# Kernel optimization log

Measured on AMD Instinct MI355X. Metric: run time of the kernel, lower is better.

The kernel has to match this reference:

```python
import jax, jax.numpy as jnp
import numpy as np

N_HEADS = 8
NODE_DIM, EDGE_DIM, TIME_DIM = 172, 172, 100
OUT_DIM = NODE_DIM + TIME_DIM  # 272, divisible by N_HEADS -> pad_dim = 0
HEAD_DIM = OUT_DIM // N_HEADS  # 34
KEY_DIM = NODE_DIM + EDGE_DIM + TIME_DIM  # 444
B, NBR = 4096, 64
LN_EPS = 1e-5


def setup_inputs() -> dict:
    key = jax.random.key(0)
    ks = jax.random.split(key, 12)
    s = 0.02
    return {
        "node_feat": jax.random.normal(ks[0], (B, NODE_DIM), jnp.float32),
        "time_feat": jax.random.normal(ks[1], (B, 1, TIME_DIM), jnp.float32),
        "edge_feat": jax.random.normal(ks[2], (B, NBR, EDGE_DIM), jnp.float32),
        "nbr_node_feat": jax.random.normal(ks[3], (B, NBR, NODE_DIM), jnp.float32),
        "nbr_time_feat": jax.random.normal(ks[4], (B, NBR, TIME_DIM), jnp.float32),
        "nbr_mask": jax.random.randint(ks[5], (B, NBR), 0, 2, jnp.int32),
        "W_Q": jax.random.normal(ks[6], (OUT_DIM, OUT_DIM), jnp.float32) * s,
        "W_KV": jax.random.normal(ks[7], (2 * OUT_DIM, KEY_DIM), jnp.float32) * s,
        "W_O": jax.random.normal(ks[8], (OUT_DIM, OUT_DIM), jnp.float32) * s,
        "b_O": jax.random.normal(ks[9], (OUT_DIM,), jnp.float32) * s,
        "ln_gamma": jnp.ones((OUT_DIM,), jnp.float32),
        "ln_beta": jnp.zeros((OUT_DIM,), jnp.float32),
    }


def reference(node_feat, time_feat, edge_feat, nbr_node_feat, nbr_time_feat,
              nbr_mask, W_Q, W_KV, W_O, b_O, ln_gamma, ln_beta):
    # Query/residual: concat node + time features -> (B, out_dim) (L=1 squeezed)
    R = jnp.concatenate([node_feat, time_feat[:, 0, :]], axis=-1)  # (B, D)
    Q = R @ W_Q.T  # (B, D)
    # Keys/values from neighbors
    Z_in = jnp.concatenate([nbr_node_feat, edge_feat, nbr_time_feat], axis=-1)  # (B,N,key_dim)
    Z = jnp.einsum('bnk,dk->bnd', Z_in, W_KV)  # (B, N, 2D)
    K, V = Z[..., :OUT_DIM], Z[..., OUT_DIM:]
    # Split heads
    Qh = Q.reshape(B, N_HEADS, HEAD_DIM)              # (B,H,d)
    Kh = K.reshape(B, NBR, N_HEADS, HEAD_DIM)         # (B,N,H,d)
    Vh = V.reshape(B, NBR, N_HEADS, HEAD_DIM)
    # Single-query attention scores: (B,H,N)
    scores = jnp.einsum('bhd,bnhd->bhn', Qh, Kh) * (HEAD_DIM ** -0.5)
    pad = (nbr_mask == 0)[:, None, :]  # (B,1,N)
    scores = jnp.where(pad, jnp.float32(-1e10), scores)
    A = jax.nn.softmax(scores, axis=-1)  # dropout is identity in eval / p=0
    O = jnp.einsum('bhn,bnhd->bhd', A, Vh).reshape(B, OUT_DIM)
    out = O @ W_O.T + b_O
    # Residual + LayerNorm
    x = out + R
    mu = jnp.mean(x, axis=-1, keepdims=True)
    var = jnp.mean(jnp.square(x - mu), axis=-1, keepdims=True)
    return (x - mu) * jax.lax.rsqrt(var + LN_EPS) * ln_gamma + ln_beta
```

## Files before the change

### kernel.cpp

```cpp
#include <hip/hip_runtime.h>
#include <hip/hip_bf16.h>
#include <string.h>

#define NROWS    4096
#define NBR      64
#define NODE_DIM 172
#define EDGE_DIM 172
#define TIME_DIM 100
#define OUT_DIM  272
#define KEY_DIM  444
#define KPAD     448
#define QK_PAD   320
#define N_HEADS  8
#define HEAD_DIM 34

typedef __attribute__((ext_vector_type(8))) short short8_t;
typedef __attribute__((ext_vector_type(4))) float f32x4;

__device__ inline short f2b(float x) {
  unsigned u = __builtin_bit_cast(unsigned, x);
  unsigned r = (u + 0x7fffu + ((u >> 16) & 1u)) >> 16;
  return (short)r;
}

__device__ inline unsigned pk2(float lo, float hi) {
  __hip_bfloat162 h = __float22bfloat162_rn(make_float2(lo, hi));
  unsigned u;
  memcpy(&u, &h, 4);
  return u;
}

typedef const __attribute__((address_space(1))) void gv_t;
typedef __attribute__((address_space(3))) void lv_t;
__device__ inline void gld16(const void* g, void* l) {
  __builtin_amdgcn_global_load_lds((gv_t*)g, (lv_t*)l, 16, 0, 0);
}

__device__ inline void barrier_lgkm() {
  asm volatile("s_waitcnt lgkmcnt(0)" ::: "memory");
  __builtin_amdgcn_sched_barrier(0);
  __builtin_amdgcn_s_barrier();
}

template<int ROWS, int KP, int K0>
__device__ inline void pad_rows(char* A, int t) {
  constexpr int NC8 = (KP - K0) / 4;
  constexpr int LPR = 512 / ROWS;
  int r = t / LPR;
  int j = t % LPR;
  char* Arow = A + r * (2 * KP);
  int swz = (r & 7) << 4;
  uint2 zz; zz.x = 0; zz.y = 0;
  for (int c8 = j; c8 < NC8; c8 += LPR)
    *(uint2*)(Arow + ((2 * K0 + 8 * c8) ^ swz)) = zz;
}

template<int MT, int KP, int NKK>
__device__ inline void gemm_tile(const short* __restrict__ Wrow, const char* A,
                                 int lr, int lk, f32x4* acc) {
#pragma unroll
  for (int kk = 0; kk < NKK; ++kk) {
    short8_t bfrag = *(const short8_t*)(Wrow + lr * KP + kk * 32 + lk * 8);
#pragma unroll
    for (int mt = 0; mt < MT; ++mt) {
      short8_t afrag = *(const short8_t*)(A + (mt * 16 + lr) * (2 * KP) +
                                          ((kk * 64 + lk * 16) ^ ((lr & 7) << 4)));
      acc[mt] = __builtin_amdgcn_mfma_f32_16x16x32_bf16(afrag, bfrag, acc[mt], 0, 0, 0);
    }
  }
}

__global__ void convert_w(const float* __restrict__ Wkv, const float* __restrict__ Wq,
                          const float* __restrict__ Wo, short* __restrict__ wq_b,
                          short* __restrict__ wo_b, short* __restrict__ wkt,
                          short* __restrict__ wvh) {
  int i = blockIdx.x * 256 + threadIdx.x;
  if (i < OUT_DIM * QK_PAD) {
    int r = i / QK_PAD, c = i - r * QK_PAD;
    wq_b[i] = (c < OUT_DIM) ? f2b(Wq[r * OUT_DIM + c]) : (short)0;
    wo_b[i] = (c < OUT_DIM) ? f2b(Wo[r * OUT_DIM + c]) : (short)0;
  }
  if (i < N_HEADS * 448 * 64) {
    int h = i / 28672;
    int rem = i - h * 28672;
    int n = rem >> 6, d = rem & 63;
    wkt[i] = (n < KEY_DIM && d < HEAD_DIM) ? f2b(Wkv[(h * HEAD_DIM + d) * KEY_DIM + n])
                                           : (short)0;
  }
  if (i < N_HEADS * 48 * 448) {
    int h = i / 21504;
    int rem = i - h * 21504;
    int cp = rem / 448, k = rem - cp * 448;
    wvh[i] = (cp < HEAD_DIM && k < KEY_DIM)
                 ? f2b(Wkv[(OUT_DIM + h * HEAD_DIM + cp) * KEY_DIM + k])
                 : (short)0;
  }
}

__global__ __launch_bounds__(512) void q_qt(const float* __restrict__ node_feat,
                                            const float* __restrict__ time_feat,
                                            const short* __restrict__ Wq,
                                            const short* __restrict__ Wkt,
                                            short* __restrict__ Qtg) {
  __shared__ char Rlds[16 * 640];
  __shared__ char Qp[16 * 1024];
  int rb = blockIdx.x * 16, t = threadIdx.x;
  {
    int r = t >> 5, j = t & 31;
    const float4* pn = (const float4*)(node_feat + (size_t)(rb + r) * NODE_DIM);
    const float4* pt = (const float4*)(time_feat + (size_t)(rb + r) * TIME_DIM);
    float4 vn[2], vt4;
    int in_[2], it_;
#pragma unroll
    for (int i = 0; i < 2; ++i) { int f = j + 32 * i; in_[i] = f > 42 ? 42 : f; vn[i] = pn[in_[i]]; }
    it_ = j > 24 ? 24 : j; vt4 = pt[it_];
    char* Arow = Rlds + r * 640;
    int swz = (r & 7) << 4;
#pragma unroll
    for (int i = 0; i < 2; ++i) {
      uint2 w; w.x = pk2(vn[i].x, vn[i].y); w.y = pk2(vn[i].z, vn[i].w);
      *(uint2*)(Arow + ((8 * in_[i]) ^ swz)) = w;
    }
    {
      uint2 w; w.x = pk2(vt4.x, vt4.y); w.y = pk2(vt4.z, vt4.w);
      *(uint2*)(Arow + ((344 + 8 * it_) ^ swz)) = w;
    }
    if (j < 12) { uint2 zz; zz.x = 0; zz.y = 0; *(uint2*)(Arow + ((544 + 8 * j) ^ swz)) = zz; }
  }
  {
    uint4 zz; zz.x = 0; zz.y = 0; zz.z = 0; zz.w = 0;
    for (int i = t; i < 1024; i += 512) ((uint4*)Qp)[i] = zz;
  }
  __syncthreads();
  int wave = t >> 6, lane = t & 63, lr = lane & 15, lk = lane >> 4;
  f32x4 z = {0.f, 0.f, 0.f, 0.f};

  for (int nt = wave; nt < 17; nt += 8) {
    int nb = nt * 16;
    f32x4 acc[1] = {z};
    gemm_tile<1, QK_PAD, QK_PAD / 32>(Wq + nb * QK_PAD, Rlds, lr, lk, acc);
    int c = nb + lr;
    int h = c / HEAD_DIM, d = c - h * HEAD_DIM;
#pragma unroll
    for (int e = 0; e < 4; ++e) {
      int r = lk * 4 + e;
      *(short*)(Qp + r * 1024 + h * 128 + ((2 * d) ^ ((r & 7) << 4))) = f2b(acc[0][e]);
    }
  }
  __syncthreads();

  int h = wave;
  const short* Wh = Wkt + h * 28672;
  for (int nt = 0; nt < 28; ++nt) {
    f32x4 acc = z;
#pragma unroll
    for (int kk = 0; kk < 2; ++kk) {
      short8_t bfrag = *(const short8_t*)(Wh + (nt * 16 + lr) * 64 + kk * 32 + lk * 8);
      short8_t afrag = *(const short8_t*)(Qp + lr * 1024 + h * 128 +
                                          ((kk * 64 + lk * 16) ^ ((lr & 7) << 4)));
      acc = __builtin_amdgcn_mfma_f32_16x16x32_bf16(afrag, bfrag, acc, 0, 0, 0);
    }
#pragma unroll
    for (int e = 0; e < 4; ++e) {
      int n = nt * 16 + lr;
      *(short*)((char*)Qtg + (size_t)(rb + lk * 4 + e) * 7168 + h * 896 +
                ((2 * n) ^ (h << 4))) = f2b(acc[e] * 0.17149858514250882f);
    }
  }
}

__device__ inline void stage_chunk(const float* __restrict__ nn,
                                   const float* __restrict__ ef,
                                   const float* __restrict__ tf,
                                   const short* __restrict__ Qtg,
                                   int b, int half, char* buf, char* qtslot, char* dump,
                                   int wave, int lane) {
  size_t row0 = (size_t)b * NBR + half * 32;
  const char* nb = (const char*)(nn + row0 * NODE_DIM);
  const char* eb = (const char*)(ef + row0 * EDGE_DIM);
  const char* tb = (const char*)(tf + row0 * TIME_DIM);
  const char* qb = (const char*)Qtg + (size_t)b * 7168;
#pragma unroll
  for (int i = 0; i < 8; ++i) {
    int q = wave * 8 + i;
    if (q < 22) {
      int off = q * 1024 + lane * 16; if (off > 22000) off = 22000;
      gld16(nb + off, buf + q * 1024);
    } else if (q < 44) {
      int off = (q - 22) * 1024 + lane * 16; if (off > 22000) off = 22000;
      gld16(eb + off, buf + 22528 + (q - 22) * 1024);
    } else if (q < 57) {
      int off = (q - 44) * 1024 + lane * 16; if (off > 12784) off = 12784;
      gld16(tb + off, buf + 45056 + (q - 44) * 1024);
    } else {
      int off = (q - 57) * 1024 + lane * 16;
      gld16(qb + off, half == 0 ? (qtslot + (q - 57) * 1024) : dump);
    }
  }
}

__global__ __launch_bounds__(512) void attn7(const float* __restrict__ nn,
                                             const float* __restrict__ ef,
                                             const float* __restrict__ tf,
                                             const int* __restrict__ nbr_mask,
                                             const short* __restrict__ Qtg,
                                             short* __restrict__ Yh2) {
  __shared__ char Zbuf[2][58368];
  __shared__ char QtS[2][7168];
  __shared__ char Dump[1024];
  __shared__ float Spart[4][32][8];
  __shared__ char Pb[16 * 64];
  __shared__ float Mh[8], Lh[8], Fh[8];
  __shared__ int Mlds[1024];
  int t = threadIdx.x;
  int wave = t >> 6, lane = t & 63, lr = lane & 15, lk = lane >> 4;
  int bbase = blockIdx.x * 16;
  f32x4 z = {0.f, 0.f, 0.f, 0.f};
  f32x4 accY[4] = {z, z, z, z};

  if (t < 256) ((int4*)Mlds)[t] = ((const int4*)(nbr_mask + (size_t)bbase * 64))[t];
  stage_chunk(nn, ef, tf, Qtg, bbase, 0, Zbuf[0], QtS[0], Dump, wave, lane);

  for (int ci = 0; ci < 32; ++ci) {
    int b = bbase + (ci >> 1), half = ci & 1;
    char* cur = Zbuf[ci & 1];

    if (ci < 31) {
      int b2 = bbase + ((ci + 1) >> 1);
      stage_chunk(nn, ef, tf, Qtg, b2, (ci + 1) & 1, Zbuf[(ci + 1) & 1], QtS[b2 & 1],
                  Dump, wave, lane);
      asm volatile("s_waitcnt vmcnt(8) lgkmcnt(0)" ::: "memory");
    } else {
      asm volatile("s_waitcnt vmcnt(0) lgkmcnt(0)" ::: "memory");
    }
    __builtin_amdgcn_sched_barrier(0);
    __builtin_amdgcn_s_barrier();

    int r = t >> 4, j = t & 15;
    f32x4 v[7];
#pragma unroll
    for (int i = 0; i < 7; ++i) {
      int k = j * 4 + i * 64;
      int off = (k < 172) ? (r * 688 + 4 * k)
              : (k < 344) ? (22528 + r * 688 + 4 * (k - 172))
                          : (45056 + r * 400 + 4 * (k - 344));
      v[i] = *(const f32x4*)(cur + off);
    }
    if (j == 15) { v[6][0] = 0.f; v[6][1] = 0.f; v[6][2] = 0.f; v[6][3] = 0.f; }
    barrier_lgkm();
    {
      char* Arow = cur + r * 896;
      int swz = (r & 7) << 4;
#pragma unroll
      for (int i = 0; i < 7; ++i) {
        uint2 w; w.x = pk2(v[i][0], v[i][1]); w.y = pk2(v[i][2], v[i][3]);
        *(uint2*)(Arow + ((8 * j + 128 * i) ^ swz)) = w;
      }
    }
    barrier_lgkm();

    {
      int ntl = wave & 1, kq = wave >> 1;
      int tb0 = kq < 2 ? kq * 4 : 8 + (kq - 2) * 3;
      int cnt = kq < 2 ? 4 : 3;
      f32x4 acc = z;
      const char* qbase = QtS[b & 1] + (lr & 7) * 896;
      const char* zbase = cur + (ntl * 16 + lr) * 896;
      int swz = (lr & 7) << 4;
      for (int it = 0; it < cnt; ++it) {
        int keb = 2 * ((tb0 + it) * 32 + lk * 8);
        short8_t a = *(const short8_t*)(qbase + (keb ^ swz));
        short8_t bb = *(const short8_t*)(zbase + (keb ^ swz));
        acc = __builtin_amdgcn_mfma_f32_16x16x32_bf16(a, bb, acc, 0, 0, 0);
      }
#pragma unroll
      for (int e = 0; e < 4; ++e) {
        int h = lk * 4 + e;
        if (h < 8) Spart[kq][ntl * 16 + lr][h] = acc[e];
      }
    }
    barrier_lgkm();

    {
      int h = wave, n = lane & 31;
      float s = Spart[0][n][h] + Spart[1][n][h] + Spart[2][n][h] + Spart[3][n][h];
      if (Mlds[(ci >> 1) * 64 + half * 32 + n] == 0) s = -1e10f;
      float m = s;
#pragma unroll
      for (int off = 16; off >= 1; off >>= 1) m = fmaxf(m, __shfl_xor(m, off));
      float mp = (half == 0) ? -3e38f : Mh[h];
      float mn = fmaxf(mp, m);
      float e = __expf(s - mn);
      float sum = e;
#pragma unroll
      for (int off = 16; off >= 1; off >>= 1) sum += __shfl_xor(sum, off);
      float f = __expf(mp - mn);
      if (lane == 0) {
        Lh[h] = (half ? Lh[h] : 0.f) * f + sum;
        Mh[h] = mn;
        Fh[h] = f;
      }
      int off2 = (2 * n) ^ ((h & 3) << 4);
      *(short*)(Pb + h * 64 + off2) = f2b(e);
      *(short*)(Pb + (h + 8) * 64 + off2) = 0;
    }
    barrier_lgkm();

    {
      short8_t pa = *(const short8_t*)(Pb + lr * 64 + ((lk * 16) ^ ((lr & 3) << 4)));
#pragma unroll
      for (int s7 = 0; s7 < 4; ++s7) {
        int vt = wave + 8 * s7;
        if (vt < 28) {
          int colb = 2 * (vt * 16 + lr);
          const char* zb_base = cur + (lk * 8) * 896;
          short8_t zb;
#pragma unroll
          for (int jx = 0; jx < 8; ++jx)
            zb[jx] = *(const short*)(zb_base + jx * 896 + (colb ^ (jx << 4)));
#pragma unroll
          for (int e = 0; e < 4; ++e) accY[s7][e] *= Fh[(lk * 4 + e) & 7];
          accY[s7] = __builtin_amdgcn_mfma_f32_16x16x32_bf16(pa, zb, accY[s7], 0, 0, 0);
        }
      }
      if (half == 1 && lk < 2) {
        float inv[4];
#pragma unroll
        for (int e = 0; e < 4; ++e) inv[e] = 1.f / Lh[lk * 4 + e];
#pragma unroll
        for (int s7 = 0; s7 < 4; ++s7) {
          int vt = wave + 8 * s7;
          if (vt < 28) {
            int k = vt * 16 + lr, kk2 = k >> 5, kp = k & 31;
#pragma unroll
            for (int e = 0; e < 4; ++e)
              Yh2[((size_t)((lk * 4 + e) * 14 + kk2) * 4096 + b) * 32 + kp] =
                  f2b(accY[s7][e] * inv[e]);
          }
        }
      }
    }
    __builtin_amdgcn_s_barrier();
  }
}

__global__ __launch_bounds__(512) void out_ln2(const short* __restrict__ Yh2,
                                               const short* __restrict__ Wvh,
                                               const short* __restrict__ Wo,
                                               const float* __restrict__ bO,
                                               const float* __restrict__ node_feat,
                                               const float* __restrict__ time_feat,
                                               const float* __restrict__ gamma,
                                               const float* __restrict__ beta,
                                               float* __restrict__ out) {
  __shared__ char Alds[16 * 640];
  __shared__ float X[16 * 276];
  int rb = blockIdx.x * 16;
  int t = threadIdx.x;
  int wave = t >> 6, lane = t & 63, lr = lane & 15, lk = lane >> 4;
  pad_rows<16, QK_PAD, OUT_DIM>(Alds, t);
  f32x4 z = {0.f, 0.f, 0.f, 0.f};

  for (int p = wave; p < 24; p += 8) {
    int h = p / 3, nt = p - h * 3;
    f32x4 acc = z;
#pragma unroll
    for (int kk = 0; kk < 14; ++kk) {
      short8_t bfrag = *(const short8_t*)(Wvh + h * 21504 + (nt * 16 + lr) * 448 +
                                          kk * 32 + lk * 8);
      short8_t afrag = *(const short8_t*)(
          Yh2 + ((size_t)(h * 14 + kk) * 4096 + rb + lr) * 32 + lk * 8);
      acc = __builtin_amdgcn_mfma_f32_16x16x32_bf16(afrag, bfrag, acc, 0, 0, 0);
    }
    int cl = nt * 16 + lr;
    if (cl < HEAD_DIM) {
      int c = h * HEAD_DIM + cl;
#pragma unroll
      for (int e = 0; e < 4; ++e) {
        int r = lk * 4 + e;
        *(short*)(Alds + r * 640 + ((2 * c) ^ ((r & 7) << 4))) = f2b(acc[e]);
      }
    }
  }
  __syncthreads();

  for (int nt = wave; nt < 17; nt += 8) {
    int nb = nt * 16;
    f32x4 acc[1] = {z};
    gemm_tile<1, QK_PAD, QK_PAD / 32>(Wo + nb * QK_PAD, Alds, lr, lk, acc);
    int c = nb + lr;
    float bo = bO[c];
#pragma unroll
    for (int e = 0; e < 4; ++e) {
      int r = lk * 4 + e;
      int gr = rb + r;
      float Rv = (c < NODE_DIM) ? node_feat[(size_t)gr * NODE_DIM + c]
                                : time_feat[(size_t)gr * TIME_DIM + (c - NODE_DIM)];
      X[r * 276 + c] = acc[0][e] + bo + Rv;
    }
  }
  __syncthreads();

  int row = t >> 5, j = t & 31;
  float s1 = 0.f, s2 = 0.f;
  for (int c = j; c < OUT_DIM; c += 32) {
    float v = X[row * 276 + c];
    s1 += v; s2 += v * v;
  }
#pragma unroll
  for (int off = 16; off >= 1; off >>= 1) {
    s1 += __shfl_xor(s1, off);
    s2 += __shfl_xor(s2, off);
  }
  float mu = s1 * (1.f / OUT_DIM);
  float var = s2 * (1.f / OUT_DIM) - mu * mu;
  float inv = rsqrtf(fmaxf(var, 0.f) + 1e-5f);
  int gr = rb + row;
  for (int c = j; c < OUT_DIM; c += 32) {
    float v = X[row * 276 + c];
    out[(size_t)gr * OUT_DIM + c] = (v - mu) * inv * gamma[c] + beta[c];
  }
}

extern "C" void kernel_launch(void* const* d_in, const int* in_sizes, int n_in,
                              void* d_out, int out_size, void* d_ws, size_t ws_size,
                              hipStream_t stream) {
  const float* node_feat = (const float*)d_in[0];
  const float* time_feat = (const float*)d_in[1];
  const float* edge_feat = (const float*)d_in[2];
  const float* nbr_node  = (const float*)d_in[3];
  const float* nbr_time  = (const float*)d_in[4];
  const int*   nbr_mask  = (const int*)d_in[5];
  const float* W_Q   = (const float*)d_in[6];
  const float* W_KV  = (const float*)d_in[7];
  const float* W_O   = (const float*)d_in[8];
  const float* b_O   = (const float*)d_in[9];
  const float* gamma = (const float*)d_in[10];
  const float* beta  = (const float*)d_in[11];
  float* out = (float*)d_out;
  char* ws = (char*)d_ws;

  short* wq_b = (short*)(ws);
  short* wo_b = (short*)(ws + 174080);
  short* wvh  = (short*)(ws + 348160);
  short* wkt  = (short*)(ws + 692224);
  short* Qtg  = (short*)(ws + 1150976);
  short* Yh2  = (short*)(ws + 30511104);

  convert_w<<<896, 256, 0, stream>>>(W_KV, W_Q, W_O, wq_b, wo_b, wkt, wvh);
  q_qt<<<NROWS / 16, 512, 0, stream>>>(node_feat, time_feat, wq_b, wkt, Qtg);
  attn7<<<256, 512, 0, stream>>>(nbr_node, edge_feat, nbr_time, nbr_mask, Qtg, Yh2);
  out_ln2<<<NROWS / 16, 512, 0, stream>>>(Yh2, wvh, wo_b, b_O, node_feat, time_feat,
                                          gamma, beta, out);
}
```

Before: 198.8 us.

## Replace persistent double-buffered attention kernel with one block per batch row

Replaces the persistent 256-block attention kernel, which double-buffered neighbor chunks and Qt tiles in LDS, with a 4096-block kernel that loads each half-chunk synchronously into a single LDS buffer. Qt is now stored unswizzled in global memory and read directly in the score MFMA loop, and the mask is read per lane from global. This cuts LDS use and may let more blocks share a CU, relying on occupancy rather than explicit prefetch to hide load latency. In exchange it gives up the intra-block load/compute overlap and adds global reads in the inner loop.

Result: faster. 190.0 us (-4.4%).

```diff
diff --git a/kernel.cpp b/kernel.cpp
--- a/kernel.cpp
+++ b/kernel.cpp
@@ -9,7 +9,6 @@
 #define TIME_DIM 100
 #define OUT_DIM  272
 #define KEY_DIM  444
-#define KPAD     448
 #define QK_PAD   320
 #define N_HEADS  8
 #define HEAD_DIM 34
@@ -34,12 +33,6 @@
 typedef __attribute__((address_space(3))) void lv_t;
 __device__ inline void gld16(const void* g, void* l) {
   __builtin_amdgcn_global_load_lds((gv_t*)g, (lv_t*)l, 16, 0, 0);
-}
-
-__device__ inline void barrier_lgkm() {
-  asm volatile("s_waitcnt lgkmcnt(0)" ::: "memory");
-  __builtin_amdgcn_sched_barrier(0);
-  __builtin_amdgcn_s_barrier();
 }
 
 template<int ROWS, int KP, int K0>
@@ -161,95 +154,66 @@
       acc = __builtin_amdgcn_mfma_f32_16x16x32_bf16(afrag, bfrag, acc, 0, 0, 0);
     }
 #pragma unroll
-    for (int e = 0; e < 4; ++e) {
-      int n = nt * 16 + lr;
-      *(short*)((char*)Qtg + (size_t)(rb + lk * 4 + e) * 7168 + h * 896 +
-                ((2 * n) ^ (h << 4))) = f2b(acc[e] * 0.17149858514250882f);
-    }
-  }
-}
-
-__device__ inline void stage_chunk(const float* __restrict__ nn,
-                                   const float* __restrict__ ef,
-                                   const float* __restrict__ tf,
-                                   const short* __restrict__ Qtg,
-                                   int b, int half, char* buf, char* qtslot, char* dump,
-                                   int wave, int lane) {
-  size_t row0 = (size_t)b * NBR + half * 32;
-  const char* nb = (const char*)(nn + row0 * NODE_DIM);
-  const char* eb = (const char*)(ef + row0 * EDGE_DIM);
-  const char* tb = (const char*)(tf + row0 * TIME_DIM);
-  const char* qb = (const char*)Qtg + (size_t)b * 7168;
-#pragma unroll
-  for (int i = 0; i < 8; ++i) {
-    int q = wave * 8 + i;
-    if (q < 22) {
-      int off = q * 1024 + lane * 16; if (off > 22000) off = 22000;
-      gld16(nb + off, buf + q * 1024);
-    } else if (q < 44) {
-      int off = (q - 22) * 1024 + lane * 16; if (off > 22000) off = 22000;
-      gld16(eb + off, buf + 22528 + (q - 22) * 1024);
-    } else if (q < 57) {
-      int off = (q - 44) * 1024 + lane * 16; if (off > 12784) off = 12784;
-      gld16(tb + off, buf + 45056 + (q - 44) * 1024);
-    } else {
-      int off = (q - 57) * 1024 + lane * 16;
-      gld16(qb + off, half == 0 ? (qtslot + (q - 57) * 1024) : dump);
-    }
-  }
-}
-
-__global__ __launch_bounds__(512) void attn7(const float* __restrict__ nn,
+    for (int e = 0; e < 4; ++e)
+      Qtg[(size_t)(rb + lk * 4 + e) * 3584 + h * 448 + nt * 16 + lr] =
+          f2b(acc[e] * 0.17149858514250882f);
+  }
+}
+
+__global__ __launch_bounds__(512) void attn8(const float* __restrict__ nn,
                                              const float* __restrict__ ef,
                                              const float* __restrict__ tf,
                                              const int* __restrict__ nbr_mask,
                                              const short* __restrict__ Qtg,
                                              short* __restrict__ Yh2) {
-  __shared__ char Zbuf[2][58368];
-  __shared__ char QtS[2][7168];
-  __shared__ char Dump[1024];
+  __shared__ char Zb[58368];
   __shared__ float Spart[4][32][8];
   __shared__ char Pb[16 * 64];
   __shared__ float Mh[8], Lh[8], Fh[8];
-  __shared__ int Mlds[1024];
+  int b = blockIdx.x;
   int t = threadIdx.x;
   int wave = t >> 6, lane = t & 63, lr = lane & 15, lk = lane >> 4;
-  int bbase = blockIdx.x * 16;
   f32x4 z = {0.f, 0.f, 0.f, 0.f};
   f32x4 accY[4] = {z, z, z, z};
 
-  if (t < 256) ((int4*)Mlds)[t] = ((const int4*)(nbr_mask + (size_t)bbase * 64))[t];
-  stage_chunk(nn, ef, tf, Qtg, bbase, 0, Zbuf[0], QtS[0], Dump, wave, lane);
-
-  for (int ci = 0; ci < 32; ++ci) {
-    int b = bbase + (ci >> 1), half = ci & 1;
-    char* cur = Zbuf[ci & 1];
-
-    if (ci < 31) {
-      int b2 = bbase + ((ci + 1) >> 1);
-      stage_chunk(nn, ef, tf, Qtg, b2, (ci + 1) & 1, Zbuf[(ci + 1) & 1], QtS[b2 & 1],
-                  Dump, wave, lane);
-      asm volatile("s_waitcnt vmcnt(8) lgkmcnt(0)" ::: "memory");
-    } else {
-      asm volatile("s_waitcnt vmcnt(0) lgkmcnt(0)" ::: "memory");
-    }
-    __builtin_amdgcn_sched_barrier(0);
-    __builtin_amdgcn_s_barrier();
-
-    int r = t >> 4, j = t & 15;
-    f32x4 v[7];
-#pragma unroll
-    for (int i = 0; i < 7; ++i) {
-      int k = j * 4 + i * 64;
-      int off = (k < 172) ? (r * 688 + 4 * k)
-              : (k < 344) ? (22528 + r * 688 + 4 * (k - 172))
-                          : (45056 + r * 400 + 4 * (k - 344));
-      v[i] = *(const f32x4*)(cur + off);
-    }
-    if (j == 15) { v[6][0] = 0.f; v[6][1] = 0.f; v[6][2] = 0.f; v[6][3] = 0.f; }
-    barrier_lgkm();
-    {
-      char* Arow = cur + r * 896;
+  int mp0 = nbr_mask[(size_t)b * NBR + (lane & 31)];
+  int mp1 = nbr_mask[(size_t)b * NBR + 32 + (lane & 31)];
+
+  for (int half = 0; half < 2; ++half) {
+    {
+      size_t row0 = (size_t)b * NBR + half * 32;
+      const char* nb = (const char*)(nn + row0 * NODE_DIM);
+      const char* eb = (const char*)(ef + row0 * EDGE_DIM);
+      const char* tb = (const char*)(tf + row0 * TIME_DIM);
+      for (int q = wave; q < 57; q += 8) {
+        if (q < 22) {
+          int off = q * 1024 + lane * 16; if (off > 22000) off = 22000;
+          gld16(nb + off, Zb + q * 1024);
+        } else if (q < 44) {
+          int off = (q - 22) * 1024 + lane * 16; if (off > 22000) off = 22000;
+          gld16(eb + off, Zb + 22528 + (q - 22) * 1024);
+        } else {
+          int off = (q - 44) * 1024 + lane * 16; if (off > 12784) off = 12784;
+          gld16(tb + off, Zb + 45056 + (q - 44) * 1024);
+        }
+      }
+    }
+    __syncthreads();
+
+    {
+      int r = t >> 4, j = t & 15;
+      f32x4 v[7];
+#pragma unroll
+      for (int i = 0; i < 7; ++i) {
+        int k = j * 4 + i * 64;
+        int off = (k < 172) ? (r * 688 + 4 * k)
+                : (k < 344) ? (22528 + r * 688 + 4 * (k - 172))
+                            : (45056 + r * 400 + 4 * (k - 344));
+        v[i] = *(const f32x4*)(Zb + off);
+      }
+      if (j == 15) { v[6][0] = 0.f; v[6][1] = 0.f; v[6][2] = 0.f; v[6][3] = 0.f; }
+      __syncthreads();
+      char* Arow = Zb + r * 896;
       int swz = (r & 7) << 4;
 #pragma unroll
       for (int i = 0; i < 7; ++i) {
@@ -257,20 +221,20 @@
         *(uint2*)(Arow + ((8 * j + 128 * i) ^ swz)) = w;
       }
     }
-    barrier_lgkm();
+    __syncthreads();
 
     {
       int ntl = wave & 1, kq = wave >> 1;
       int tb0 = kq < 2 ? kq * 4 : 8 + (kq - 2) * 3;
       int cnt = kq < 2 ? 4 : 3;
       f32x4 acc = z;
-      const char* qbase = QtS[b & 1] + (lr & 7) * 896;
-      const char* zbase = cur + (ntl * 16 + lr) * 896;
+      const short* qrow = Qtg + (size_t)b * 3584 + (lr & 7) * 448;
+      const char* zbase = Zb + (ntl * 16 + lr) * 896;
       int swz = (lr & 7) << 4;
       for (int it = 0; it < cnt; ++it) {
-        int keb = 2 * ((tb0 + it) * 32 + lk * 8);
-        short8_t a = *(const short8_t*)(qbase + (keb ^ swz));
-        short8_t bb = *(const short8_t*)(zbase + (keb ^ swz));
+        int ke = (tb0 + it) * 32 + lk * 8;
+        short8_t a = *(const short8_t*)(qrow + ke);
+        short8_t bb = *(const short8_t*)(zbase + ((2 * ke) ^ swz));
         acc = __builtin_amdgcn_mfma_f32_16x16x32_bf16(a, bb, acc, 0, 0, 0);
       }
 #pragma unroll
@@ -279,12 +243,13 @@
         if (h < 8) Spart[kq][ntl * 16 + lr][h] = acc[e];
       }
     }
-    barrier_lgkm();
+    __syncthreads();
 
     {
       int h = wave, n = lane & 31;
       float s = Spart[0][n][h] + Spart[1][n][h] + Spart[2][n][h] + Spart[3][n][h];
-      if (Mlds[(ci >> 1) * 64 + half * 32 + n] == 0) s = -1e10f;
+      int mw = (half == 0) ? mp0 : mp1;
+      if (mw == 0) s = -1e10f;
       float m = s;
 #pragma unroll
       for (int off = 16; off >= 1; off >>= 1) m = fmaxf(m, __shfl_xor(m, off));
@@ -304,7 +269,7 @@
       *(short*)(Pb + h * 64 + off2) = f2b(e);
       *(short*)(Pb + (h + 8) * 64 + off2) = 0;
     }
-    barrier_lgkm();
+    __syncthreads();
 
     {
       short8_t pa = *(const short8_t*)(Pb + lr * 64 + ((lk * 16) ^ ((lr & 3) << 4)));
@@ -313,34 +278,35 @@
         int vt = wave + 8 * s7;
         if (vt < 28) {
           int colb = 2 * (vt * 16 + lr);
-          const char* zb_base = cur + (lk * 8) * 896;
-          short8_t zb;
+          const char* zb_base = Zb + (lk * 8) * 896;
+          short8_t zbv;
 #pragma unroll
           for (int jx = 0; jx < 8; ++jx)
-            zb[jx] = *(const short*)(zb_base + jx * 896 + (colb ^ (jx << 4)));
+            zbv[jx] = *(const short*)(zb_base + jx * 896 + (colb ^ (jx << 4)));
 #pragma unroll
           for (int e = 0; e < 4; ++e) accY[s7][e] *= Fh[(lk * 4 + e) & 7];
-          accY[s7] = __builtin_amdgcn_mfma_f32_16x16x32_bf16(pa, zb, accY[s7], 0, 0, 0);
+          accY[s7] = __builtin_amdgcn_mfma_f32_16x16x32_bf16(pa, zbv, accY[s7], 0, 0, 0);
         }
       }
-      if (half == 1 && lk < 2) {
-        float inv[4];
-#pragma unroll
-        for (int e = 0; e < 4; ++e) inv[e] = 1.f / Lh[lk * 4 + e];
-#pragma unroll
-        for (int s7 = 0; s7 < 4; ++s7) {
-          int vt = wave + 8 * s7;
-          if (vt < 28) {
-            int k = vt * 16 + lr, kk2 = k >> 5, kp = k & 31;
-#pragma unroll
-            for (int e = 0; e < 4; ++e)
-              Yh2[((size_t)((lk * 4 + e) * 14 + kk2) * 4096 + b) * 32 + kp] =
-                  f2b(accY[s7][e] * inv[e]);
-          }
-        }
-      }
-    }
-    __builtin_amdgcn_s_barrier();
+    }
+    __syncthreads();
+  }
+
+  if (lk < 2) {
+    float inv[4];
+#pragma unroll
+    for (int e = 0; e < 4; ++e) inv[e] = 1.f / Lh[lk * 4 + e];
+#pragma unroll
+    for (int s7 = 0; s7 < 4; ++s7) {
+      int vt = wave + 8 * s7;
+      if (vt < 28) {
+        int k = vt * 16 + lr, kk2 = k >> 5, kp = k & 31;
+#pragma unroll
+        for (int e = 0; e < 4; ++e)
+          Yh2[((size_t)((lk * 4 + e) * 14 + kk2) * 4096 + b) * 32 + kp] =
+              f2b(accY[s7][e] * inv[e]);
+      }
+    }
   }
 }
 
@@ -449,7 +415,7 @@
 
   convert_w<<<896, 256, 0, stream>>>(W_KV, W_Q, W_O, wq_b, wo_b, wkt, wvh);
   q_qt<<<NROWS / 16, 512, 0, stream>>>(node_feat, time_feat, wq_b, wkt, Qtg);
-  attn7<<<256, 512, 0, stream>>>(nbr_node, edge_feat, nbr_time, nbr_mask, Qtg, Yh2);
+  attn8<<<NROWS, 512, 0, stream>>>(nbr_node, edge_feat, nbr_time, nbr_mask, Qtg, Yh2);
   out_ln2<<<NROWS / 16, 512, 0, stream>>>(Yh2, wvh, wo_b, b_O, node_feat, time_feat,
                                           gamma, beta, out);
 }
```
